# Performance work log

Hardware: AMD Instinct MI355X
Metric: run time of the kernel (lower is better)

The kernel has to match this reference:

```python
import jax, jax.numpy as jnp
import numpy as np


def setup_inputs() -> dict:
    key = jax.random.key(0)
    ks = jax.random.split(key, 6)
    B = 65536
    x = jax.random.normal(ks[0], (B, 784), dtype=jnp.float32)
    conv_w = jax.random.normal(ks[1], (3, 3), dtype=jnp.float32)
    fc1_w = jax.random.normal(ks[2], (100, 676), dtype=jnp.float32) * (1.0 / np.sqrt(676))
    fc1_b = jax.random.normal(ks[3], (100,), dtype=jnp.float32) * 0.01
    fc2_w = jax.random.normal(ks[4], (10, 100), dtype=jnp.float32) * (1.0 / np.sqrt(100))
    fc2_b = jax.random.normal(ks[5], (10,), dtype=jnp.float32) * 0.01
    return {"x": x, "conv_w": conv_w, "fc1_w": fc1_w, "fc1_b": fc1_b, "fc2_w": fc2_w, "fc2_b": fc2_b}


def reference(x, conv_w, fc1_w, fc1_b, fc2_w, fc2_b):
    B = x.shape[0]
    img = x.reshape(B, 1, 28, 28)  # NCHW, single channel
    kern = conv_w.reshape(1, 1, 3, 3)  # OIHW
    # 'valid' cross-correlation, matching the slicing-based Convolve()
    conv = jax.lax.conv_general_dilated(
        img, kern, window_strides=(1, 1), padding='VALID',
        dimension_numbers=('NCHW', 'OIHW', 'NCHW'))  # [B,1,26,26]
    h = conv.reshape(B, 26 * 26)
    h = jax.nn.relu(h @ fc1_w.T + fc1_b)
    out = h @ fc2_w.T + fc2_b
    return out
```

## Files before the change

### kernel.cpp

```cpp
#include <hip/hip_runtime.h>


typedef short  s16x8 __attribute__((ext_vector_type(8)));
typedef float  f32x4 __attribute__((ext_vector_type(4)));

#define BM   32
#define XP   808
#define HSTR 132
#define NT   8
#define KC   25

__device__ __forceinline__ unsigned short f2bf_rtne(float f) {
    unsigned int u = __builtin_bit_cast(unsigned int, f);
    u = (u + 0x7fffu + ((u >> 16) & 1u)) >> 16;
    return (unsigned short)u;
}

extern "C" __global__ void __launch_bounds__(256)
prep_w1eff(const float* __restrict__ W1, const float* __restrict__ cw9,
           const float* __restrict__ b1, unsigned short* __restrict__ bw)
{
    int id = blockIdx.x * 256 + threadIdx.x;
    if (id >= NT * KC * 64) return;
    int lane = id & 63;
    int kc   = (id >> 6) % KC;
    int t    = id / (KC * 64);
    int n    = t * 16 + (lane & 15);
    int k0   = kc * 32 + (lane >> 4) * 8;

    float cw[9];
#pragma unroll
    for (int i = 0; i < 9; ++i) cw[i] = cw9[i];

    unsigned short v[8];
#pragma unroll
    for (int j = 0; j < 8; ++j) {
        int k = k0 + j;
        float f = 0.f;
        if (n < 100) {
            if (k < 784) {
                int i = k / 28, jj = k % 28;
                for (int dr = 0; dr < 3; ++dr)
                    for (int dc = 0; dc < 3; ++dc) {
                        int a = i - dr, b = jj - dc;
                        if (a >= 0 && a < 26 && b >= 0 && b < 26)
                            f = fmaf(W1[(size_t)n * 676 + a * 26 + b],
                                     cw[dr * 3 + dc], f);
                    }
            } else if (k == 784) {
                f = b1[n];
            }
        }
        v[j] = f2bf_rtne(f);
    }
    *(uint4*)(bw + (size_t)id * 8) = *(const uint4*)v;
}

template<int NTILES>
__device__ __forceinline__ void gemm_loop(
    const unsigned short* arow0, const unsigned short* arow1,
    const uint4* __restrict__ bwv, int t0, int t1, int lane,
    f32x4& acc00, f32x4& acc01, f32x4& acc10, f32x4& acc11)
{
    uint4 b0v[3], b1v[3];
#pragma unroll
    for (int i = 0; i < 3; ++i) {
        b0v[i] = bwv[(t0 * KC + i) * 64 + lane];
        if (NTILES == 2) b1v[i] = bwv[(t1 * KC + i) * 64 + lane];
    }
    uint4 a0 = *(const uint4*)(arow0);
    uint4 a1 = *(const uint4*)(arow1);
#pragma unroll
    for (int kc = 0; kc < KC; ++kc) {
        uint4 cb0 = b0v[kc % 3];
        uint4 cb1 = (NTILES == 2) ? b1v[kc % 3] : cb0;
        if (kc + 3 < KC) {
            b0v[kc % 3] = bwv[(t0 * KC + kc + 3) * 64 + lane];
            if (NTILES == 2) b1v[kc % 3] = bwv[(t1 * KC + kc + 3) * 64 + lane];
        }
        uint4 na0 = a0, na1 = a1;
        if (kc + 1 < KC) {
            na0 = *(const uint4*)(arow0 + (kc + 1) * 32);
            na1 = *(const uint4*)(arow1 + (kc + 1) * 32);
        }
        s16x8 av0 = __builtin_bit_cast(s16x8, a0);
        s16x8 av1 = __builtin_bit_cast(s16x8, a1);
        acc00 = __builtin_amdgcn_mfma_f32_16x16x32_bf16(
            av0, __builtin_bit_cast(s16x8, cb0), acc00, 0, 0, 0);
        acc10 = __builtin_amdgcn_mfma_f32_16x16x32_bf16(
            av1, __builtin_bit_cast(s16x8, cb0), acc10, 0, 0, 0);
        if (NTILES == 2) {
            acc01 = __builtin_amdgcn_mfma_f32_16x16x32_bf16(
                av0, __builtin_bit_cast(s16x8, cb1), acc01, 0, 0, 0);
            acc11 = __builtin_amdgcn_mfma_f32_16x16x32_bf16(
                av1, __builtin_bit_cast(s16x8, cb1), acc11, 0, 0, 0);
        }
        a0 = na0; a1 = na1;
    }
}

extern "C" __global__ void __launch_bounds__(256, 3)
digit_gemm(const float* __restrict__ x,
           const unsigned short* __restrict__ bw,
           const float* __restrict__ W2,
           const float* __restrict__ b2,
           float* __restrict__ out)
{
    __shared__ __align__(16) unsigned char smem[BM * XP * 2];
    unsigned short* xbuf = (unsigned short*)smem;
    float*          hbuf = (float*)smem;

    const int tid  = threadIdx.x;
    const int lane = tid & 63;
    const int wv   = tid >> 6;
    const int q    = lane >> 4;
    const int mn   = lane & 15;
    const int m0   = blockIdx.x * BM;

    {
        int mi = tid >> 3, u = tid & 7;
        *(unsigned int*)(xbuf + mi * XP + 784 + u * 2) = (u == 0) ? 0x3F80u : 0u;
    }

    const float4* xg = (const float4*)(x + (size_t)m0 * 784);
    for (int rr = 0; rr < 3; ++rr) {
        float4 v[8];
#pragma unroll
        for (int i = 0; i < 8; ++i)
            v[i] = xg[tid + 256 * (rr * 8 + i)];
#pragma unroll
        for (int i = 0; i < 8; ++i) {
            int g  = tid + 256 * (rr * 8 + i);
            int mi = g / 196, c4 = g - mi * 196;
            unsigned int ax = __builtin_bit_cast(unsigned int, v[i].x) + 0x8000u;
            unsigned int ay = __builtin_bit_cast(unsigned int, v[i].y) + 0x8000u;
            unsigned int az = __builtin_bit_cast(unsigned int, v[i].z) + 0x8000u;
            unsigned int aw = __builtin_bit_cast(unsigned int, v[i].w) + 0x8000u;
            uint2 w;
            w.x = (ax >> 16) | (ay & 0xffff0000u);
            w.y = (az >> 16) | (aw & 0xffff0000u);
            *(uint2*)(xbuf + mi * XP + c4 * 4) = w;
        }
    }
    if (tid < 128) {
        int g  = 6144 + tid;
        float4 vv = xg[g];
        int mi = g / 196, c4 = g - mi * 196;
        unsigned int ax = __builtin_bit_cast(unsigned int, vv.x) + 0x8000u;
        unsigned int ay = __builtin_bit_cast(unsigned int, vv.y) + 0x8000u;
        unsigned int az = __builtin_bit_cast(unsigned int, vv.z) + 0x8000u;
        unsigned int aw = __builtin_bit_cast(unsigned int, vv.w) + 0x8000u;
        uint2 w;
        w.x = (ax >> 16) | (ay & 0xffff0000u);
        w.y = (az >> 16) | (aw & 0xffff0000u);
        *(uint2*)(xbuf + mi * XP + c4 * 4) = w;
    }
    __syncthreads();

    f32x4 acc00, acc01, acc10, acc11;
#pragma unroll
    for (int i = 0; i < 4; ++i) { acc00[i]=0.f; acc01[i]=0.f; acc10[i]=0.f; acc11[i]=0.f; }

    const unsigned short* arow0 = xbuf + mn * XP + q * 8;
    const unsigned short* arow1 = xbuf + (16 + mn) * XP + q * 8;
    const uint4* bwv = (const uint4*)bw;
    const int t0 = wv, t1 = wv + 4;

    if (wv < 3)
        gemm_loop<2>(arow0, arow1, bwv, t0, t1, lane, acc00, acc01, acc10, acc11);
    else
        gemm_loop<1>(arow0, arow1, bwv, t0, t1, lane, acc00, acc01, acc10, acc11);
    __syncthreads();

#pragma unroll
    for (int r = 0; r < 4; ++r) {
        int row = q * 4 + r;
        float v;
        v = acc00[r]; v = v > 0.f ? v : 0.f; hbuf[ row       * HSTR + t0 * 16 + mn] = v;
        v = acc10[r]; v = v > 0.f ? v : 0.f; hbuf[(row + 16) * HSTR + t0 * 16 + mn] = v;
        if (wv < 3) {
            v = acc01[r]; v = v > 0.f ? v : 0.f; hbuf[ row       * HSTR + t1 * 16 + mn] = v;
            v = acc11[r]; v = v > 0.f ? v : 0.f; hbuf[(row + 16) * HSTR + t1 * 16 + mn] = v;
        }
    }
    __syncthreads();

    for (int p = tid; p < BM * 10; p += 256) {
        int mi = p / 10, o = p - mi * 10;
        const float4* hv = (const float4*)(hbuf + mi * HSTR);
        const float4* w2 = (const float4*)(W2 + (size_t)o * 100);
        float s = b2[o];
#pragma unroll
        for (int g = 0; g < 25; ++g) {
            float4 h4 = hv[g], w4 = w2[g];
            s += h4.x*w4.x + h4.y*w4.y + h4.z*w4.z + h4.w*w4.w;
        }
        out[(size_t)(m0 + mi) * 10 + o] = s;
    }
}

extern "C" void kernel_launch(void* const* d_in, const int* in_sizes, int n_in,
                              void* d_out, int out_size, void* d_ws, size_t ws_size,
                              hipStream_t stream) {
    const float* x  = (const float*)d_in[0];
    const float* cw = (const float*)d_in[1];
    const float* W1 = (const float*)d_in[2];
    const float* b1 = (const float*)d_in[3];
    const float* W2 = (const float*)d_in[4];
    const float* b2 = (const float*)d_in[5];
    float* out = (float*)d_out;
    unsigned short* bw = (unsigned short*)d_ws;

    const int B = in_sizes[0] / 784;

    hipLaunchKernelGGL(prep_w1eff, dim3((NT * KC * 64 + 255) / 256), dim3(256),
                       0, stream, W1, cw, b1, bw);
    hipLaunchKernelGGL(digit_gemm, dim3(B / BM), dim3(256), 0, stream,
                       x, bw, W2, b2, out);
}
```

Measured before the change: 321.7 us.

## Make digit GEMM persistent with register-resident weights and double-buffered input prefetch

Launches a fixed grid of 256 persistent blocks, each looping over several 32-row tiles. Each wave keeps its W1-effective B fragments in registers for the whole kernel, stages W2 in LDS, and prefetches the next tile's x into registers while the current tile's MFMA runs, then writes it to a second LDS buffer. The aim is to hide global-load latency and stop reloading weights per tile. In exchange, register pressure rises sharply (about 50 uint4 plus 25 float4 per thread) and occupancy falls to one block per CU, and the grid assumes B divides evenly into 256 blocks of tiles.

```diff
diff --git a/kernel.cpp b/kernel.cpp
--- a/kernel.cpp
+++ b/kernel.cpp
@@ -9,6 +9,7 @@
 #define HSTR 132
 #define NT   8
 #define KC   25
+#define GRID 256
 
 __device__ __forceinline__ unsigned short f2bf_rtne(float f) {
     unsigned int u = __builtin_bit_cast(unsigned int, f);
@@ -56,146 +57,182 @@
     *(uint4*)(bw + (size_t)id * 8) = *(const uint4*)v;
 }
 
+#define MFMA(a, b, c) __builtin_amdgcn_mfma_f32_16x16x32_bf16(a, b, c, 0, 0, 0)
+
 template<int NTILES>
-__device__ __forceinline__ void gemm_loop(
+__device__ __forceinline__ void compute_tile(
     const unsigned short* arow0, const unsigned short* arow1,
-    const uint4* __restrict__ bwv, int t0, int t1, int lane,
+    const uint4 (&br0)[KC], const uint4 (&br1)[KC],
     f32x4& acc00, f32x4& acc01, f32x4& acc10, f32x4& acc11)
 {
-    uint4 b0v[3], b1v[3];
-#pragma unroll
-    for (int i = 0; i < 3; ++i) {
-        b0v[i] = bwv[(t0 * KC + i) * 64 + lane];
-        if (NTILES == 2) b1v[i] = bwv[(t1 * KC + i) * 64 + lane];
-    }
-    uint4 a0 = *(const uint4*)(arow0);
-    uint4 a1 = *(const uint4*)(arow1);
 #pragma unroll
     for (int kc = 0; kc < KC; ++kc) {
-        uint4 cb0 = b0v[kc % 3];
-        uint4 cb1 = (NTILES == 2) ? b1v[kc % 3] : cb0;
-        if (kc + 3 < KC) {
-            b0v[kc % 3] = bwv[(t0 * KC + kc + 3) * 64 + lane];
-            if (NTILES == 2) b1v[kc % 3] = bwv[(t1 * KC + kc + 3) * 64 + lane];
-        }
-        uint4 na0 = a0, na1 = a1;
-        if (kc + 1 < KC) {
-            na0 = *(const uint4*)(arow0 + (kc + 1) * 32);
-            na1 = *(const uint4*)(arow1 + (kc + 1) * 32);
-        }
+        uint4 a0 = *(const uint4*)(arow0 + kc * 32);
+        uint4 a1 = *(const uint4*)(arow1 + kc * 32);
         s16x8 av0 = __builtin_bit_cast(s16x8, a0);
         s16x8 av1 = __builtin_bit_cast(s16x8, a1);
-        acc00 = __builtin_amdgcn_mfma_f32_16x16x32_bf16(
-            av0, __builtin_bit_cast(s16x8, cb0), acc00, 0, 0, 0);
-        acc10 = __builtin_amdgcn_mfma_f32_16x16x32_bf16(
-            av1, __builtin_bit_cast(s16x8, cb0), acc10, 0, 0, 0);
+        s16x8 bv0 = __builtin_bit_cast(s16x8, br0[kc]);
+        acc00 = MFMA(av0, bv0, acc00);
+        acc10 = MFMA(av1, bv0, acc10);
         if (NTILES == 2) {
-            acc01 = __builtin_amdgcn_mfma_f32_16x16x32_bf16(
-                av0, __builtin_bit_cast(s16x8, cb1), acc01, 0, 0, 0);
-            acc11 = __builtin_amdgcn_mfma_f32_16x16x32_bf16(
-                av1, __builtin_bit_cast(s16x8, cb1), acc11, 0, 0, 0);
-        }
-        a0 = na0; a1 = na1;
-    }
-}
-
-extern "C" __global__ void __launch_bounds__(256, 3)
+            s16x8 bv1 = __builtin_bit_cast(s16x8, br1[kc]);
+            acc01 = MFMA(av0, bv1, acc01);
+            acc11 = MFMA(av1, bv1, acc11);
+        }
+    }
+}
+
+__device__ __forceinline__ void bar_lds() {
+    asm volatile("s_waitcnt lgkmcnt(0)" ::: "memory");
+    __builtin_amdgcn_s_barrier();
+}
+
+__device__ __forceinline__ void cvt_store(unsigned short* dst, float4 f) {
+    unsigned int ax = __builtin_bit_cast(unsigned int, f.x) + 0x8000u;
+    unsigned int ay = __builtin_bit_cast(unsigned int, f.y) + 0x8000u;
+    unsigned int az = __builtin_bit_cast(unsigned int, f.z) + 0x8000u;
+    unsigned int aw = __builtin_bit_cast(unsigned int, f.w) + 0x8000u;
+    uint2 w;
+    w.x = (ax >> 16) | (ay & 0xffff0000u);
+    w.y = (az >> 16) | (aw & 0xffff0000u);
+    *(uint2*)dst = w;
+}
+
+extern "C" __global__ void __launch_bounds__(256, 1)
 digit_gemm(const float* __restrict__ x,
            const unsigned short* __restrict__ bw,
            const float* __restrict__ W2,
            const float* __restrict__ b2,
-           float* __restrict__ out)
+           float* __restrict__ out,
+           int ntiles)
 {
-    __shared__ __align__(16) unsigned char smem[BM * XP * 2];
-    unsigned short* xbuf = (unsigned short*)smem;
-    float*          hbuf = (float*)smem;
+    __shared__ __align__(16) unsigned short xbuf[2][BM * XP];
+    __shared__ __align__(16) float w2buf[10 * 100];
+    __shared__ __align__(16) float hbuf[BM * HSTR];
 
     const int tid  = threadIdx.x;
     const int lane = tid & 63;
     const int wv   = tid >> 6;
     const int q    = lane >> 4;
     const int mn   = lane & 15;
-    const int m0   = blockIdx.x * BM;
+    const int tile0 = blockIdx.x * ntiles;
+
+    const uint4* bwv = (const uint4*)bw;
+    const int t0 = wv, t1 = wv + 4;
+    uint4 br0[KC], br1[KC];
+#pragma unroll
+    for (int kc = 0; kc < KC; ++kc) {
+        br0[kc] = bwv[(t0 * KC + kc) * 64 + lane];
+        br1[kc] = bwv[(t1 * KC + kc) * 64 + lane];
+    }
+
+#pragma unroll
+    for (int i = 0; i < 4; ++i) {
+        int j = tid + 256 * i;
+        if (j < 1000) w2buf[j] = W2[j];
+    }
+    const int p0 = tid,      mi0 = p0 / 10, o0 = p0 - mi0 * 10;
+    const int p1 = tid + 256;
+    const bool has1 = (p1 < BM * 10);
+    const int mi1 = p1 / 10, o1 = p1 - mi1 * 10;
+    const float bb0 = b2[o0];
+    const float bb1 = has1 ? b2[o1] : 0.f;
 
     {
         int mi = tid >> 3, u = tid & 7;
-        *(unsigned int*)(xbuf + mi * XP + 784 + u * 2) = (u == 0) ? 0x3F80u : 0u;
-    }
-
-    const float4* xg = (const float4*)(x + (size_t)m0 * 784);
-    for (int rr = 0; rr < 3; ++rr) {
-        float4 v[8];
-#pragma unroll
-        for (int i = 0; i < 8; ++i)
-            v[i] = xg[tid + 256 * (rr * 8 + i)];
-#pragma unroll
-        for (int i = 0; i < 8; ++i) {
-            int g  = tid + 256 * (rr * 8 + i);
-            int mi = g / 196, c4 = g - mi * 196;
-            unsigned int ax = __builtin_bit_cast(unsigned int, v[i].x) + 0x8000u;
-            unsigned int ay = __builtin_bit_cast(unsigned int, v[i].y) + 0x8000u;
-            unsigned int az = __builtin_bit_cast(unsigned int, v[i].z) + 0x8000u;
-            unsigned int aw = __builtin_bit_cast(unsigned int, v[i].w) + 0x8000u;
-            uint2 w;
-            w.x = (ax >> 16) | (ay & 0xffff0000u);
-            w.y = (az >> 16) | (aw & 0xffff0000u);
-            *(uint2*)(xbuf + mi * XP + c4 * 4) = w;
-        }
-    }
-    if (tid < 128) {
-        int g  = 6144 + tid;
-        float4 vv = xg[g];
-        int mi = g / 196, c4 = g - mi * 196;
-        unsigned int ax = __builtin_bit_cast(unsigned int, vv.x) + 0x8000u;
-        unsigned int ay = __builtin_bit_cast(unsigned int, vv.y) + 0x8000u;
-        unsigned int az = __builtin_bit_cast(unsigned int, vv.z) + 0x8000u;
-        unsigned int aw = __builtin_bit_cast(unsigned int, vv.w) + 0x8000u;
-        uint2 w;
-        w.x = (ax >> 16) | (ay & 0xffff0000u);
-        w.y = (az >> 16) | (aw & 0xffff0000u);
-        *(uint2*)(xbuf + mi * XP + c4 * 4) = w;
-    }
-    __syncthreads();
-
-    f32x4 acc00, acc01, acc10, acc11;
-#pragma unroll
-    for (int i = 0; i < 4; ++i) { acc00[i]=0.f; acc01[i]=0.f; acc10[i]=0.f; acc11[i]=0.f; }
-
-    const unsigned short* arow0 = xbuf + mn * XP + q * 8;
-    const unsigned short* arow1 = xbuf + (16 + mn) * XP + q * 8;
-    const uint4* bwv = (const uint4*)bw;
-    const int t0 = wv, t1 = wv + 4;
-
-    if (wv < 3)
-        gemm_loop<2>(arow0, arow1, bwv, t0, t1, lane, acc00, acc01, acc10, acc11);
-    else
-        gemm_loop<1>(arow0, arow1, bwv, t0, t1, lane, acc00, acc01, acc10, acc11);
-    __syncthreads();
-
-#pragma unroll
-    for (int r = 0; r < 4; ++r) {
-        int row = q * 4 + r;
-        float v;
-        v = acc00[r]; v = v > 0.f ? v : 0.f; hbuf[ row       * HSTR + t0 * 16 + mn] = v;
-        v = acc10[r]; v = v > 0.f ? v : 0.f; hbuf[(row + 16) * HSTR + t0 * 16 + mn] = v;
-        if (wv < 3) {
-            v = acc01[r]; v = v > 0.f ? v : 0.f; hbuf[ row       * HSTR + t1 * 16 + mn] = v;
-            v = acc11[r]; v = v > 0.f ? v : 0.f; hbuf[(row + 16) * HSTR + t1 * 16 + mn] = v;
-        }
-    }
-    __syncthreads();
-
-    for (int p = tid; p < BM * 10; p += 256) {
-        int mi = p / 10, o = p - mi * 10;
-        const float4* hv = (const float4*)(hbuf + mi * HSTR);
-        const float4* w2 = (const float4*)(W2 + (size_t)o * 100);
-        float s = b2[o];
-#pragma unroll
-        for (int g = 0; g < 25; ++g) {
-            float4 h4 = hv[g], w4 = w2[g];
-            s += h4.x*w4.x + h4.y*w4.y + h4.z*w4.z + h4.w*w4.w;
-        }
-        out[(size_t)(m0 + mi) * 10 + o] = s;
+        unsigned int pv = (u == 0) ? 0x3F80u : 0u;
+        *(unsigned int*)(&xbuf[0][mi * XP + 784 + u * 2]) = pv;
+        *(unsigned int*)(&xbuf[1][mi * XP + 784 + u * 2]) = pv;
+    }
+
+    {
+        const float4* xg = (const float4*)(x + (size_t)tile0 * BM * 784);
+        float4 v[25];
+#pragma unroll
+        for (int i = 0; i < 24; ++i) v[i] = xg[tid + 256 * i];
+        if (tid < 128) v[24] = xg[6144 + tid];
+#pragma unroll
+        for (int i = 0; i < 25; ++i) {
+            if (i < 24 || tid < 128) {
+                int g = tid + 256 * i;
+                int mi = g / 196, c4 = g - mi * 196;
+                cvt_store(&xbuf[0][mi * XP + c4 * 4], v[i]);
+            }
+        }
+    }
+    bar_lds();
+
+    for (int t = 0; t < ntiles; ++t) {
+        const int cur = t & 1;
+        const int m0  = (tile0 + t) * BM;
+
+        float4 v[25];
+        const bool more = (t + 1 < ntiles);
+        if (more) {
+            const float4* xg = (const float4*)(x + (size_t)(tile0 + t + 1) * BM * 784);
+#pragma unroll
+            for (int i = 0; i < 24; ++i) v[i] = xg[tid + 256 * i];
+            if (tid < 128) v[24] = xg[6144 + tid];
+        }
+
+        f32x4 acc00, acc01, acc10, acc11;
+#pragma unroll
+        for (int i = 0; i < 4; ++i) { acc00[i]=0.f; acc01[i]=0.f; acc10[i]=0.f; acc11[i]=0.f; }
+        const unsigned short* arow0 = &xbuf[cur][mn * XP + q * 8];
+        const unsigned short* arow1 = &xbuf[cur][(16 + mn) * XP + q * 8];
+        if (wv < 3)
+            compute_tile<2>(arow0, arow1, br0, br1, acc00, acc01, acc10, acc11);
+        else
+            compute_tile<1>(arow0, arow1, br0, br1, acc00, acc01, acc10, acc11);
+
+#pragma unroll
+        for (int r = 0; r < 4; ++r) {
+            int row = q * 4 + r;
+            float z;
+            z = acc00[r]; z = z > 0.f ? z : 0.f; hbuf[ row       * HSTR + t0 * 16 + mn] = z;
+            z = acc10[r]; z = z > 0.f ? z : 0.f; hbuf[(row + 16) * HSTR + t0 * 16 + mn] = z;
+            if (wv < 3) {
+                z = acc01[r]; z = z > 0.f ? z : 0.f; hbuf[ row       * HSTR + t1 * 16 + mn] = z;
+                z = acc11[r]; z = z > 0.f ? z : 0.f; hbuf[(row + 16) * HSTR + t1 * 16 + mn] = z;
+            }
+        }
+        bar_lds();
+
+        {
+            const float4* hv = (const float4*)(hbuf + mi0 * HSTR);
+            const float4* w2 = (const float4*)(w2buf + o0 * 100);
+            float s = bb0;
+#pragma unroll
+            for (int g = 0; g < 25; ++g) {
+                float4 h4 = hv[g], w4 = w2[g];
+                s += h4.x*w4.x + h4.y*w4.y + h4.z*w4.z + h4.w*w4.w;
+            }
+            out[(size_t)(m0 + mi0) * 10 + o0] = s;
+        }
+        if (has1) {
+            const float4* hv = (const float4*)(hbuf + mi1 * HSTR);
+            const float4* w2 = (const float4*)(w2buf + o1 * 100);
+            float s = bb1;
+#pragma unroll
+            for (int g = 0; g < 25; ++g) {
+                float4 h4 = hv[g], w4 = w2[g];
+                s += h4.x*w4.x + h4.y*w4.y + h4.z*w4.z + h4.w*w4.w;
+            }
+            out[(size_t)(m0 + mi1) * 10 + o1] = s;
+        }
+
+        if (more) {
+            unsigned short* xb = &xbuf[cur ^ 1][0];
+#pragma unroll
+            for (int i = 0; i < 25; ++i) {
+                if (i < 24 || tid < 128) {
+                    int g = tid + 256 * i;
+                    int mi = g / 196, c4 = g - mi * 196;
+                    cvt_store(xb + mi * XP + c4 * 4, v[i]);
+                }
+            }
+        }
+        bar_lds();
     }
 }
 
@@ -212,9 +249,10 @@
     unsigned short* bw = (unsigned short*)d_ws;
 
     const int B = in_sizes[0] / 784;
+    const int ntiles = (B / BM) / GRID;
 
     hipLaunchKernelGGL(prep_w1eff, dim3((NT * KC * 64 + 255) / 256), dim3(256),
                        0, stream, W1, cw, b1, bw);
-    hipLaunchKernelGGL(digit_gemm, dim3(B / BM), dim3(256), 0, stream,
-                       x, bw, W2, b2, out);
-}
+    hipLaunchKernelGGL(digit_gemm, dim3(GRID), dim3(256), 0, stream,
+                       x, bw, W2, b2, out, ntiles);
+}
```

New measurement: 317.7 us. About the same (-1.2%).
